# Optimization experiments

Hardware: AMD Instinct MI355X
Metric: run time of the kernel (lower is better)

## Reference

```python
import jax, jax.numpy as jnp
import numpy as np

BN_EPS = 1e-5
ITER_N = 5

def _bn(x, gamma, beta, mean, var, axis):
    shape = [1] * x.ndim
    shape[axis] = -1
    r = lambda v: v.reshape(shape)
    return (x - r(mean)) * (r(gamma) / jnp.sqrt(r(var) + BN_EPS)) + r(beta)

def _covpool(x):
    # x: (B, d, M); MPNCOV CovpoolLayer: y = x @ I_hat @ x^T, I_hat = (1/M)I - (1/M^2)11^T
    M = x.shape[-1]
    I_hat = (-1.0 / (M * M)) * jnp.ones((M, M), x.dtype) + (1.0 / M) * jnp.eye(M, dtype=x.dtype)
    return jnp.einsum('bdm,mn,ben->bde', x, I_hat, x)

def _sqrtm_ns(A, iterN=ITER_N):
    # MPNCOV SqrtmLayer: trace-normalized Newton-Schulz iteration
    d = A.shape[-1]
    I3 = 3.0 * jnp.eye(d, dtype=A.dtype)
    normA = jnp.trace(A, axis1=1, axis2=2) / 3.0          # (B,)
    A_n = A / normA[:, None, None]
    ZY = 0.5 * (I3 - A_n)
    Y = A_n @ ZY
    Z = ZY
    for _ in range(iterN - 2):
        ZY = 0.5 * (I3 - Z @ Y)
        Y = Y @ ZY
        Z = ZY @ Z
    YZY = 0.5 * (Y @ (I3 - Z @ Y))
    return YZY * jnp.sqrt(normA)[:, None, None]

def setup_inputs() -> dict:
    key = jax.random.key(0)
    ks = jax.random.split(key, 12)
    B, C, H, W = 64, 1024, 16, 16
    D, R = 128, H * W  # att_dim, sp_reso
    return {
        'x': jax.random.normal(ks[0], (B, C, H, W), jnp.float32),
        'w_dr': jax.random.normal(ks[1], (D, C), jnp.float32) * 0.02,
        'b_dr': jax.random.normal(ks[2], (D,), jnp.float32) * 0.02,
        'bn1_gamma': jnp.ones((D,), jnp.float32),
        'bn1_beta': jnp.zeros((D,), jnp.float32),
        'bn1_mean': jax.random.normal(ks[3], (D,), jnp.float32) * 0.1,
        'bn1_var': jax.random.uniform(ks[4], (D,), jnp.float32, 0.5, 1.5),
        'bn2_gamma': jnp.ones((R,), jnp.float32),
        'bn2_beta': jnp.zeros((R,), jnp.float32),
        'bn2_mean': jax.random.normal(ks[5], (R,), jnp.float32) * 0.1,
        'bn2_var': jax.random.uniform(ks[6], (R,), jnp.float32, 0.5, 1.5),
        'rc_w': jax.random.normal(ks[7], (R,), jnp.float32) * 0.1 + 1.0,
        'rc_b': jax.random.normal(ks[8], (R,), jnp.float32) * 0.02,
        'fc_w': jax.random.normal(ks[9], (R, R * R), jnp.float32) * 0.004,
        'fc_b': jax.random.normal(ks[10], (R,), jnp.float32) * 0.02,
    }

def reference(x, w_dr, b_dr, bn1_gamma, bn1_beta, bn1_mean, bn1_var,
              bn2_gamma, bn2_beta, bn2_mean, bn2_var, rc_w, rc_b, fc_w, fc_b):
    B, C, H, W = x.shape
    # 1x1 dimension-reduction conv + BN + ReLU
    y = jnp.einsum('bchw,dc->bdhw', x, w_dr) + b_dr[None, :, None, None]
    y = jax.nn.relu(_bn(y, bn1_gamma, bn1_beta, bn1_mean, bn1_var, axis=1))
    # (B, D, HW) -> (B, HW, D): HW spatial positions as 'channels', D as samples
    y = y.reshape(B, -1, H * W).transpose(0, 2, 1)
    cov = _covpool(y)                  # (B, HW, HW)
    s = _sqrtm_ns(cov, ITER_N)         # (B, HW, HW)
    # row BN over first HW axis (channels of the (B, HW, HW, 1) view)
    s = _bn(s, bn2_gamma, bn2_beta, bn2_mean, bn2_var, axis=1)
    # grouped (depthwise) 1x1 row conv: per-row scale + bias
    s = s * rc_w[None, :, None] + rc_b[None, :, None]
    att = jax.nn.sigmoid(s.reshape(B, -1) @ fc_w.T + fc_b)   # (B, HW)
    att = att.reshape(B, 1, H, W)
    return x * att
```

## Files before the change

### kernel.cpp

```cpp
#include <hip/hip_runtime.h>

typedef unsigned short u16;
typedef unsigned int   u32;
typedef __attribute__((ext_vector_type(8))) short bf8;
typedef __attribute__((ext_vector_type(4))) float f4;
typedef __attribute__((ext_vector_type(16))) float f16f;

#define MFMA(a,b,c)   __builtin_amdgcn_mfma_f32_16x16x32_bf16(a,b,c,0,0,0)
#define MFMA32(a,b,c) __builtin_amdgcn_mfma_f32_32x32x16_bf16(a,b,c,0,0,0)

__device__ __forceinline__ u16 f2bf(float f){
  u32 u = __float_as_uint(f);
  u += 0x7fffu + ((u >> 16) & 1u);
  return (u16)(u >> 16);
}
__device__ __forceinline__ float bf2f(u16 h){ return __uint_as_float(((u32)h) << 16); }
__device__ __forceinline__ u32 pk2(float a, float b){ return (u32)f2bf(a) | ((u32)f2bf(b) << 16); }

__device__ __forceinline__ bf8 ldsFrag(const char* m, int row0, int k0, int pitch){
  int l = threadIdx.x & 63;
  int r = row0 + (l & 15);
  int kb = ((k0 + ((l >> 4) << 3)) << 1) ^ ((r & 7) << 4);
  return *(const bf8*)(m + r * pitch + kb);
}
__device__ __forceinline__ void ldsPut(char* m, int row, int col, int pitch, u16 v){
  int kb = (col << 1) ^ ((row & 7) << 4);
  *(u16*)(m + row * pitch + kb) = v;
}

__device__ __forceinline__ bf8 fragNS(const char* m, int r0, int ks, int l){
  int r = r0 + (l & 31);
  int kb = ((ks << 5) + ((l >> 5) << 4)) ^ ((r & 15) << 4);
  return *(const bf8*)(m + r * 256 + kb);
}
__device__ __forceinline__ bf8 fragWT(const char* m, int r0, int ks, int l){
  int r = r0 + (l & 31);
  int kb = ((ks << 5) + ((l >> 5) << 4)) ^ ((r & 15) << 4);
  return *(const bf8*)(m + r * 512 + kb);
}
__device__ __forceinline__ char* nsAddr(char* m, int row, int col4){
  return m + row * 256 + ((col4 << 1) ^ ((row & 15) << 4));
}

__device__ __forceinline__ void mmPass(const char* A, const char* B, f16f (&acc)[2][2],
                                       int R0, int C0, int l){
  #pragma unroll
  for (int ks = 0; ks < 8; ++ks){
    bf8 a0 = fragNS(A, R0,      ks, l);
    bf8 a1 = fragNS(A, R0 + 32, ks, l);
    bf8 b0 = fragNS(B, C0,      ks, l);
    bf8 b1 = fragNS(B, C0 + 32, ks, l);
    acc[0][0] = MFMA32(a0, b0, acc[0][0]); acc[0][1] = MFMA32(a0, b1, acc[0][1]);
    acc[1][0] = MFMA32(a1, b0, acc[1][0]); acc[1][1] = MFMA32(a1, b1, acc[1][1]);
  }
}

__device__ __forceinline__ void writeTile(char* D, const f16f (&acc)[2][2], int R0, int C0, int l,
                                          float scale, float dval, const uint2* adv){
  #pragma unroll
  for (int ri = 0; ri < 2; ++ri)
  #pragma unroll
  for (int ci = 0; ci < 2; ++ci)
  #pragma unroll
  for (int g = 0; g < 4; ++g){
    int srow = C0 + ci * 32 + (l & 31);
    int scol = R0 + ri * 32 + g * 8 + ((l >> 5) << 2);
    float v[4];
    #pragma unroll
    for (int q = 0; q < 4; ++q){
      float x = scale * acc[ri][ci][g * 4 + q];
      x += ((scol + q) == srow) ? dval : 0.f;
      v[q] = x;
    }
    if (adv){
      uint2 ad = adv[(ri * 2 + ci) * 4 + g];
      v[0] += 1.5f * bf2f((u16)ad.x);
      v[1] += 1.5f * bf2f((u16)(ad.x >> 16));
      v[2] += 1.5f * bf2f((u16)ad.y);
      v[3] += 1.5f * bf2f((u16)(ad.y >> 16));
    }
    *(uint2*)nsAddr(D, srow, scol) = make_uint2(pk2(v[0], v[1]), pk2(v[2], v[3]));
  }
}

__global__ void k_zero(float* __restrict__ p){
  int i = blockIdx.x * 256 + threadIdx.x;
  if (i < 16384) p[i] = 0.f;
}

__global__ __launch_bounds__(512) void k_conv(
    const float* __restrict__ x, const float* __restrict__ wdr, const float* __restrict__ bdr,
    const float* __restrict__ g1, const float* __restrict__ be1,
    const float* __restrict__ m1, const float* __restrict__ v1,
    u16* __restrict__ Wg, u16* __restrict__ WTg){
  __shared__ union {
    struct { char A[16384]; char Bt[8192]; } s;
    struct { float y[128 * 65]; float musum[8 * 64]; float mu[64]; } e;
  } sm;
  int t = threadIdx.x;
  int b = blockIdx.x >> 2, hw0 = (blockIdx.x & 3) * 64;
  int w = t >> 6, l = t & 63;
  int rows0 = (w >> 1) * 32, cols0 = (w & 1) * 32;
  int lc = l & 15, lr = (l >> 4) * 4;

  const f4 fz = {0.f, 0.f, 0.f, 0.f};
  f4 acc[2][2];
  acc[0][0] = fz; acc[0][1] = fz; acc[1][0] = fz; acc[1][1] = fz;

  int ad = t >> 2;
  int ac = (t & 3) * 16;
  const float* xb = x + (size_t)b * 1024 * 256 + hw0;

  for (int kk = 0; kk < 16; ++kk) {
    int c0 = kk * 64;
    #pragma unroll
    for (int j = 0; j < 4; ++j) {
      float4 vv = *(const float4*)(wdr + (size_t)ad * 1024 + c0 + ac + j * 4);
      int cb = ((ac + j * 4) * 2) ^ ((ad & 7) << 4);
      *(u32*)(sm.s.A + ad * 128 + cb)     = pk2(vv.x, vv.y);
      *(u32*)(sm.s.A + ad * 128 + cb + 4) = pk2(vv.z, vv.w);
    }
    #pragma unroll
    for (int j2 = 0; j2 < 4; ++j2) {
      int cc = w * 8 + j2 * 2;
      float v0 = xb[(size_t)(c0 + cc) * 256 + l];
      float v1x = xb[(size_t)(c0 + cc + 1) * 256 + l];
      int cb = (cc * 2) ^ ((l & 7) << 4);
      *(u32*)(sm.s.Bt + l * 128 + cb) = pk2(v0, v1x);
    }
    __syncthreads();
    #pragma unroll
    for (int ks = 0; ks < 2; ++ks) {
      int k0 = ks * 32;
      bf8 a0 = ldsFrag(sm.s.A, rows0,      k0, 128);
      bf8 a1 = ldsFrag(sm.s.A, rows0 + 16, k0, 128);
      bf8 b0 = ldsFrag(sm.s.Bt, cols0,      k0, 128);
      bf8 b1 = ldsFrag(sm.s.Bt, cols0 + 16, k0, 128);
      acc[0][0] = MFMA(a0, b0, acc[0][0]);
      acc[0][1] = MFMA(a0, b1, acc[0][1]);
      acc[1][0] = MFMA(a1, b0, acc[1][0]);
      acc[1][1] = MFMA(a1, b1, acc[1][1]);
    }
    __syncthreads();
  }
  #pragma unroll
  for (int i = 0; i < 2; ++i)
    #pragma unroll
    for (int r = 0; r < 4; ++r) {
      int d = rows0 + i * 16 + lr + r;
      float s1 = g1[d] * rsqrtf(v1[d] + 1e-5f);
      float t1 = (bdr[d] - m1[d]) * s1 + be1[d];
      #pragma unroll
      for (int j = 0; j < 2; ++j) {
        int hwl = cols0 + j * 16 + lc;
        sm.e.y[d * 65 + hwl] = fmaxf(acc[i][j][r] * s1 + t1, 0.f);
      }
    }
  __syncthreads();
  { int part = t >> 6, col = t & 63;
    float s = 0.f;
    #pragma unroll
    for (int i2 = 0; i2 < 16; ++i2) s += sm.e.y[(part * 16 + i2) * 65 + col];
    sm.e.musum[part * 64 + col] = s;
  }
  __syncthreads();
  if (t < 64) {
    float m = 0.f;
    #pragma unroll
    for (int p = 0; p < 8; ++p) m += sm.e.musum[p * 64 + t];
    sm.e.mu[t] = m * (1.0f / 128.0f);
  }
  __syncthreads();
  const float ISM = 0.08838834764831845f;
  { int hwl = t >> 3, dc = (t & 7) * 16;
    float muv = sm.e.mu[hwl];
    u32 q[8];
    #pragma unroll
    for (int jj = 0; jj < 8; ++jj) {
      float a = (sm.e.y[(dc + 2 * jj)     * 65 + hwl] - muv) * ISM;
      float c = (sm.e.y[(dc + 2 * jj + 1) * 65 + hwl] - muv) * ISM;
      q[jj] = pk2(a, c);
    }
    uint4* d4 = (uint4*)(Wg + ((size_t)(b * 256 + hw0 + hwl) * 128 + dc));
    d4[0] = make_uint4(q[0], q[1], q[2], q[3]);
    d4[1] = make_uint4(q[4], q[5], q[6], q[7]);
  }
  { int d = t >> 2, hc = (t & 3) * 16;
    u32 q[8];
    #pragma unroll
    for (int jj = 0; jj < 8; ++jj) {
      int h0 = hc + 2 * jj, h1 = hc + 2 * jj + 1;
      float a = (sm.e.y[d * 65 + h0] - sm.e.mu[h0]) * ISM;
      float c = (sm.e.y[d * 65 + h1] - sm.e.mu[h1]) * ISM;
      q[jj] = pk2(a, c);
    }
    uint4* d4 = (uint4*)(WTg + ((size_t)(b * 128 + d) * 256 + hw0 + hc));
    d4[0] = make_uint4(q[0], q[1], q[2], q[3]);
    d4[1] = make_uint4(q[4], q[5], q[6], q[7]);
  }
}

extern __shared__ char smns[];
__global__ __launch_bounds__(512, 2) void k_ns(const u16* __restrict__ WT,
                                               u16* __restrict__ yf, float* __restrict__ normAg){
  int b = blockIdx.x, t = threadIdx.x;
  char* Yb = smns;
  char* Zb = smns + 32768;
  char* T1 = smns + 65536;
  char* T2 = smns + 98304;
  char* T3 = smns + 131072;
  char* WTl = smns + 65536;
  char* G   = T3;
  float* trp = (float*)smns;

  int w = t >> 6, l = t & 63;
  int wq = w & 3;
  int R0 = (wq >> 1) * 64, C0 = (wq & 1) * 64;

  {
    const u16* src = WT + (size_t)b * 32768;
    int row = t >> 2, q = t & 3;
    #pragma unroll
    for (int j = 0; j < 8; ++j) {
      int c16 = q + j * 4;
      bf8 v = *(const bf8*)(src + row * 256 + c16 * 8);
      int ph = c16 ^ (row & 15);
      *(bf8*)(WTl + row * 512 + ph * 16) = v;
    }
  }
  if (t == 0) *trp = 0.f;
  __syncthreads();

  int R0g = (w & 3) * 32, C0g = (w >> 2) * 64;
  const f16f fz16 = {};
  f16f gac[2]; gac[0] = fz16; gac[1] = fz16;
  #pragma unroll
  for (int ks = 0; ks < 16; ++ks){
    bf8 a  = fragWT(WTl, R0g,      ks, l);
    bf8 b0 = fragWT(WTl, C0g,      ks, l);
    bf8 b1 = fragWT(WTl, C0g + 32, ks, l);
    gac[0] = MFMA32(a, b0, gac[0]);
    gac[1] = MFMA32(a, b1, gac[1]);
  }
  float tp = 0.f;
  #pragma unroll
  for (int ci = 0; ci < 2; ++ci)
    #pragma unroll
    for (int e = 0; e < 16; ++e){
      int row = R0g + (e & 3) + 8 * (e >> 2) + ((l >> 5) << 2);
      int col = C0g + ci * 32 + (l & 31);
      if (row == col) tp += gac[ci][e];
    }
  #pragma unroll
  for (int off = 32; off > 0; off >>= 1) tp += __shfl_down(tp, off);
  if (l == 0) atomicAdd(trp, tp);
  __syncthreads();

  float normA = fmaxf(*trp / 3.0f, 1e-12f);
  if (t == 0) normAg[b] = normA;
  float inv = 1.0f / normA;
  #pragma unroll
  for (int ci = 0; ci < 2; ++ci)
    #pragma unroll
    for (int g = 0; g < 4; ++g){
      int srow = C0g + ci * 32 + (l & 31);
      int scol = R0g + g * 8 + ((l >> 5) << 2);
      float v0 = gac[ci][g * 4 + 0] * inv, v1 = gac[ci][g * 4 + 1] * inv;
      float v2 = gac[ci][g * 4 + 2] * inv, v3 = gac[ci][g * 4 + 3] * inv;
      *(uint2*)nsAddr(G, srow, scol) = make_uint2(pk2(v0, v1), pk2(v2, v3));
    }
  __syncthreads();

  bf8 gA[8], gB[8];
  #pragma unroll
  for (int ks = 0; ks < 8; ++ks){
    gA[ks] = fragNS(G, C0,      ks, l);
    gB[ks] = fragNS(G, C0 + 32, ks, l);
  }
  { int row = t >> 2, q4 = t & 3;
    #pragma unroll
    for (int j = 0; j < 4; ++j){
      int c16 = q4 * 4 + j;
      int ph = c16 ^ (row & 15);
      bf8 gg = *(const bf8*)(G + row * 256 + ph * 16);
      bf8 yv, zv;
      #pragma unroll
      for (int e = 0; e < 8; ++e){
        int col = c16 * 8 + e;
        float y = -0.5f * bf2f((u16)gg[e]) + ((col == row) ? 1.5f : 0.f);
        yv[e] = (short)f2bf(y);
        zv[e] = (col == row) ? (short)f2bf(-0.5f) : (short)0;
      }
      *(bf8*)(Yb + row * 256 + ph * 16) = yv;
      *(bf8*)(Zb + row * 256 + ph * 16) = zv;
    }
  }
  __syncthreads();

  float z0 = 1.5f;
  for (int it = 0; it < 4; ++it){
    {
      f16f acc[2][2]; acc[0][0] = fz16; acc[0][1] = fz16; acc[1][0] = fz16; acc[1][1] = fz16;
      const char* As = (w < 4) ? Zb : Yb;
      #pragma unroll
      for (int ks = 0; ks < 8; ++ks){
        bf8 a0 = fragNS(As, R0,      ks, l);
        bf8 a1 = fragNS(As, R0 + 32, ks, l);
        acc[0][0] = MFMA32(a0, gA[ks], acc[0][0]); acc[0][1] = MFMA32(a0, gB[ks], acc[0][1]);
        acc[1][0] = MFMA32(a1, gA[ks], acc[1][0]); acc[1][1] = MFMA32(a1, gB[ks], acc[1][1]);
      }
      writeTile((w < 4) ? T1 : T3, acc, R0, C0, l, 1.0f, (w < 4) ? z0 : 0.f, nullptr);
    }
    __syncthreads();

    uint2 adv[16];
    {
      const char* addsrc = (w < 4) ? Zb : Yb;
      #pragma unroll
      for (int ri = 0; ri < 2; ++ri)
      #pragma unroll
      for (int ci = 0; ci < 2; ++ci)
      #pragma unroll
      for (int g = 0; g < 4; ++g){
        int srow = C0 + ci * 32 + (l & 31);
        int scol = R0 + ri * 32 + g * 8 + ((l >> 5) << 2);
        adv[(ri * 2 + ci) * 4 + g] = *(const uint2*)nsAddr((char*)addsrc, srow, scol);
      }
      if (w < 4){
        f16f acc[2][2]; acc[0][0] = fz16; acc[0][1] = fz16; acc[1][0] = fz16; acc[1][1] = fz16;
        mmPass(T1, Yb, acc, R0, C0, l);
        writeTile(T2, acc, R0, C0, l, -0.5f, 0.f, nullptr);
      }
    }
    __syncthreads();

    if ((w >= 4) || (it < 3)){
      f16f acc[2][2]; acc[0][0] = fz16; acc[0][1] = fz16; acc[1][0] = fz16; acc[1][1] = fz16;
      const char* A3 = (w < 4) ? T2 : T3;
      const char* B3 = (w < 4) ? T1 : T2;
      mmPass(A3, B3, acc, R0, C0, l);
      writeTile((w < 4) ? Zb : Yb, acc, R0, C0, l, 1.0f, 0.f, adv);
    }
    __syncthreads();
    z0 *= 1.5f;
  }

  {
    int row = t >> 2, q = t & 3;
    u16* dst = yf + (size_t)b * 16384 + row * 128;
    #pragma unroll
    for (int j = 0; j < 4; ++j) {
      int c16 = q * 4 + j;
      int ph = c16 ^ (row & 15);
      *(bf8*)(dst + c16 * 8) = *(const bf8*)(Yb + row * 256 + ph * 16);
    }
  }
}

extern __shared__ char smex[];
__global__ __launch_bounds__(512) void k_expand(
    const u16* __restrict__ Wg, const u16* __restrict__ yf, const float* __restrict__ normAg,
    const float* __restrict__ g2, const float* __restrict__ be2, const float* __restrict__ m2,
    const float* __restrict__ v2, const float* __restrict__ rcw, const float* __restrict__ rcb,
    u16* __restrict__ sp){
  int blk = blockIdx.x, b = blk >> 2, iband = blk & 3;
  char* Bm = smex;
  char* Yl = smex + 65536;
  char* El = smex + 98304;
  int t = threadIdx.x;
  { const u16* src = Wg + (size_t)b * 32768;
    int row = t >> 1, q = t & 1;
    #pragma unroll
    for (int j = 0; j < 8; ++j) {
      int c16 = q + j * 2;
      bf8 v = *(const bf8*)(src + row * 128 + c16 * 8);
      int ph = c16 ^ (row & 7);
      *(bf8*)(Bm + row * 256 + ph * 16) = v;
    } }
  { const u16* src = yf + (size_t)b * 16384;
    int row = t >> 2, q = t & 3;
    #pragma unroll
    for (int j = 0; j < 4; ++j) {
      int c16 = q + j * 4;
      bf8 v = *(const bf8*)(src + row * 128 + c16 * 8);
      int ph = c16 ^ (row & 7);
      *(bf8*)(Yl + row * 256 + ph * 16) = v;
    } }
  __syncthreads();
  int w = t >> 6, l = t & 63, lc = l & 15, lr = (l >> 4) * 4;
  const f4 fz = {0.f, 0.f, 0.f, 0.f};
  { int r0 = (w >> 2) * 32, c0 = (w & 3) * 32;
    f4 acc[2][2];
    acc[0][0] = fz; acc[0][1] = fz; acc[1][0] = fz; acc[1][1] = fz;
    #pragma unroll
    for (int kk = 0; kk < 4; ++kk) {
      int k0 = kk * 32;
      bf8 a0 = ldsFrag(Bm, iband * 64 + r0,      k0, 256);
      bf8 a1 = ldsFrag(Bm, iband * 64 + r0 + 16, k0, 256);
      bf8 b0 = ldsFrag(Yl, c0,      k0, 256);
      bf8 b1 = ldsFrag(Yl, c0 + 16, k0, 256);
      acc[0][0] = MFMA(a0, b0, acc[0][0]); acc[0][1] = MFMA(a0, b1, acc[0][1]);
      acc[1][0] = MFMA(a1, b0, acc[1][0]); acc[1][1] = MFMA(a1, b1, acc[1][1]);
    }
    #pragma unroll
    for (int i = 0; i < 2; ++i)
      #pragma unroll
      for (int j = 0; j < 2; ++j)
        #pragma unroll
        for (int r = 0; r < 4; ++r)
          ldsPut(El, r0 + i * 16 + lr + r, c0 + j * 16 + lc, 256, f2bf(acc[i][j][r]));
  }
  __syncthreads();
  { float invs = rsqrtf(normAg[b]);
    int r0 = (w >> 2) * 32, c0 = (w & 3) * 64;
    f4 acc[2][4];
    #pragma unroll
    for (int i = 0; i < 2; ++i)
      #pragma unroll
      for (int j = 0; j < 4; ++j) acc[i][j] = fz;
    #pragma unroll
    for (int kk = 0; kk < 4; ++kk) {
      int k0 = kk * 32;
      bf8 a0 = ldsFrag(El, r0,      k0, 256);
      bf8 a1 = ldsFrag(El, r0 + 16, k0, 256);
      bf8 b0 = ldsFrag(Bm, c0,      k0, 256);
      bf8 b1 = ldsFrag(Bm, c0 + 16, k0, 256);
      bf8 b2 = ldsFrag(Bm, c0 + 32, k0, 256);
      bf8 b3 = ldsFrag(Bm, c0 + 48, k0, 256);
      acc[0][0] = MFMA(a0, b0, acc[0][0]); acc[0][1] = MFMA(a0, b1, acc[0][1]);
      acc[0][2] = MFMA(a0, b2, acc[0][2]); acc[0][3] = MFMA(a0, b3, acc[0][3]);
      acc[1][0] = MFMA(a1, b0, acc[1][0]); acc[1][1] = MFMA(a1, b1, acc[1][1]);
      acc[1][2] = MFMA(a1, b2, acc[1][2]); acc[1][3] = MFMA(a1, b3, acc[1][3]);
    }
    #pragma unroll
    for (int i = 0; i < 2; ++i)
      #pragma unroll
      for (int r = 0; r < 4; ++r) {
        int il = r0 + i * 16 + lr + r;
        int ig = iband * 64 + il;
        float bs = g2[ig] * rsqrtf(v2[ig] + 1e-5f);
        float al = bs * rcw[ig];
        float be = (be2[ig] - m2[ig] * bs) * rcw[ig] + rcb[ig];
        #pragma unroll
        for (int j = 0; j < 4; ++j) {
          int jg = c0 + j * 16 + lc;
          sp[(size_t)b * 65536 + ig * 256 + jg] = f2bf(acc[i][j][r] * invs * al + be);
        }
      }
  }
}

extern __shared__ char smfc[];
__global__ __launch_bounds__(512) void k_fc(const u16* __restrict__ sp,
                                            const float* __restrict__ fcw,
                                            float* __restrict__ logits){
  int kc = blockIdx.x >> 1, rh = blockIdx.x & 1;
  int k0 = kc * 256, rbase = rh * 128;
  char* Al = smfc;
  char* Bl = smfc + 32768;
  int t = threadIdx.x;
  { int row = t >> 3, q = t & 7;
    #pragma unroll
    for (int j = 0; j < 4; ++j) {
      int c16 = q + j * 8;
      bf8 v = *(const bf8*)(sp + (size_t)row * 65536 + k0 + c16 * 8);
      int ph = c16 ^ (row & 7);
      *(bf8*)(Al + row * 512 + ph * 16) = v;
    } }
  { int lane16 = t & 15;
    #pragma unroll
    for (int pass = 0; pass < 4; ++pass) {
      int row = (t >> 4) + pass * 32;
      #pragma unroll
      for (int j = 0; j < 4; ++j) {
        int k = lane16 * 4 + j * 64;
        float4 v = *(const float4*)(fcw + (size_t)(rbase + row) * 65536 + k0 + k);
        int off = (k * 2) ^ ((row & 7) << 4);
        *(u32*)(Bl + row * 512 + off)     = pk2(v.x, v.y);
        *(u32*)(Bl + row * 512 + off + 4) = pk2(v.z, v.w);
      }
    } }
  __syncthreads();
  int w = t >> 6, l = t & 63, lc = l & 15, lr = (l >> 4) * 4;
  int r0 = (w >> 2) * 32, c0 = (w & 3) * 32;
  const f4 fz = {0.f, 0.f, 0.f, 0.f};
  f4 acc[2][2];
  acc[0][0] = fz; acc[0][1] = fz; acc[1][0] = fz; acc[1][1] = fz;
  #pragma unroll
  for (int kk = 0; kk < 8; ++kk) {
    int ks = kk * 32;
    bf8 a0 = ldsFrag(Al, r0,      ks, 512);
    bf8 a1 = ldsFrag(Al, r0 + 16, ks, 512);
    bf8 b0 = ldsFrag(Bl, c0,      ks, 512);
    bf8 b1 = ldsFrag(Bl, c0 + 16, ks, 512);
    acc[0][0] = MFMA(a0, b0, acc[0][0]); acc[0][1] = MFMA(a0, b1, acc[0][1]);
    acc[1][0] = MFMA(a1, b0, acc[1][0]); acc[1][1] = MFMA(a1, b1, acc[1][1]);
  }
  #pragma unroll
  for (int i = 0; i < 2; ++i)
    #pragma unroll
    for (int j = 0; j < 2; ++j)
      #pragma unroll
      for (int r = 0; r < 4; ++r) {
        int row = r0 + i * 16 + lr + r;
        int col = rbase + c0 + j * 16 + lc;
        atomicAdd(logits + row * 256 + col, acc[i][j][r]);
      }
}

__global__ __launch_bounds__(256) void k_mul(const float* __restrict__ x,
                                             const float* __restrict__ logits,
                                             const float* __restrict__ fcb,
                                             float* __restrict__ out, int n4){
  int i = blockIdx.x * 256 + threadIdx.x;
  int str = gridDim.x * 256;
  for (; i < n4; i += str) {
    int e = i << 2;
    int b = e >> 18;
    int hw = e & 255;
    float4 xv = ((const float4*)x)[i];
    float4 lg = *(const float4*)(logits + (b << 8) + hw);
    float4 fb = *(const float4*)(fcb + hw);
    float4 o;
    o.x = xv.x / (1.f + expf(-(lg.x + fb.x)));
    o.y = xv.y / (1.f + expf(-(lg.y + fb.y)));
    o.z = xv.z / (1.f + expf(-(lg.z + fb.z)));
    o.w = xv.w / (1.f + expf(-(lg.w + fb.w)));
    ((float4*)out)[i] = o;
  }
}

extern "C" void kernel_launch(void* const* d_in, const int* in_sizes, int n_in,
                              void* d_out, int out_size, void* d_ws, size_t ws_size,
                              hipStream_t stream){
  const float* x   = (const float*)d_in[0];
  const float* wdr = (const float*)d_in[1];
  const float* bdr = (const float*)d_in[2];
  const float* g1  = (const float*)d_in[3];
  const float* be1 = (const float*)d_in[4];
  const float* m1  = (const float*)d_in[5];
  const float* v1  = (const float*)d_in[6];
  const float* g2  = (const float*)d_in[7];
  const float* be2 = (const float*)d_in[8];
  const float* m2  = (const float*)d_in[9];
  const float* v2  = (const float*)d_in[10];
  const float* rcw = (const float*)d_in[11];
  const float* rcb = (const float*)d_in[12];
  const float* fcw = (const float*)d_in[13];
  const float* fcb = (const float*)d_in[14];
  float* out = (float*)d_out;
  char* ws = (char*)d_ws;
  u16*   Wg  = (u16*)(ws);
  u16*   WTg = (u16*)(ws + (4u  << 20));
  u16*   yfg = (u16*)(ws + (8u  << 20));
  float* nAg = (float*)(ws + (10u << 20));
  u16*   spg = (u16*)(ws + (11u << 20));
  float* lgt = (float*)(ws + (20u << 20));

  hipFuncSetAttribute((const void*)k_ns,     hipFuncAttributeMaxDynamicSharedMemorySize, 163840);
  hipFuncSetAttribute((const void*)k_expand, hipFuncAttributeMaxDynamicSharedMemorySize, 114688);
  hipFuncSetAttribute((const void*)k_fc,     hipFuncAttributeMaxDynamicSharedMemorySize, 98304);

  k_zero  <<<64,   256, 0,      stream>>>(lgt);
  k_conv  <<<256,  512, 0,      stream>>>(x, wdr, bdr, g1, be1, m1, v1, Wg, WTg);
  k_ns    <<<64,   512, 163840, stream>>>(WTg, yfg, nAg);
  k_expand<<<256,  512, 114688, stream>>>(Wg, yfg, nAg, g2, be2, m2, v2, rcw, rcb, spg);
  k_fc    <<<512,  512, 98304,  stream>>>(spg, fcw, lgt);
  k_mul   <<<2048, 256, 0,      stream>>>(x, lgt, fcb, out, 4194304);
}
```

Measured before the change: 122.1 us.

## Pre-convert conv weights to swizzled bf16, double-buffer conv loads, halve spatial tile

A new prep kernel converts the 1x1 conv weight to bf16 in the swizzled LDS layout once per call and also zeroes the logits buffer. The conv kernel now copies those prepped weights straight into LDS and prefetches the next K-chunk of weights and input into registers while the MFMAs run on double-buffered LDS. Each block covers 32 spatial positions instead of 64, doubling the grid to 512 blocks for better CU occupancy. The cost is that every block rereads the full weight tile, and the grid adds an extra round of per-block epilogue reductions.

```diff
diff --git a/kernel.cpp b/kernel.cpp
--- a/kernel.cpp
+++ b/kernel.cpp
@@ -83,120 +83,133 @@
   }
 }
 
-__global__ void k_zero(float* __restrict__ p){
+__global__ __launch_bounds__(256) void k_prep(const float* __restrict__ wdr,
+                                              float* __restrict__ logits,
+                                              u16* __restrict__ prep){
   int i = blockIdx.x * 256 + threadIdx.x;
-  if (i < 16384) p[i] = 0.f;
+  if (i < 16384) logits[i] = 0.f;
+  #pragma unroll
+  for (int j = 0; j < 2; ++j){
+    int e = i + j * 65536;
+    int chunk = e >> 13, rem = e & 8191, d = rem >> 6, cb2 = rem & 63;
+    int c = ((cb2 * 2) ^ ((d & 7) << 4)) >> 1;
+    prep[e] = f2bf(wdr[d * 1024 + chunk * 64 + c]);
+  }
 }
 
 __global__ __launch_bounds__(512) void k_conv(
-    const float* __restrict__ x, const float* __restrict__ wdr, const float* __restrict__ bdr,
+    const u16* __restrict__ wprep, const float* __restrict__ x, const float* __restrict__ bdr,
     const float* __restrict__ g1, const float* __restrict__ be1,
     const float* __restrict__ m1, const float* __restrict__ v1,
     u16* __restrict__ Wg, u16* __restrict__ WTg){
   __shared__ union {
-    struct { char A[16384]; char Bt[8192]; } s;
-    struct { float y[128 * 65]; float musum[8 * 64]; float mu[64]; } e;
+    struct { u16 A[2][8192]; u16 Bt[2][2048]; } s;
+    struct { float y[128 * 33]; float musum[512]; float mu[32]; } e;
   } sm;
   int t = threadIdx.x;
-  int b = blockIdx.x >> 2, hw0 = (blockIdx.x & 3) * 64;
+  int b = blockIdx.x >> 3, hw0 = (blockIdx.x & 7) * 32;
+  const float* xb = x + (size_t)b * 262144 + hw0;
+
   int w = t >> 6, l = t & 63;
-  int rows0 = (w >> 1) * 32, cols0 = (w & 1) * 32;
+  int d0 = (w >> 1) * 32, hh = (w & 1) * 16;
   int lc = l & 15, lr = (l >> 4) * 4;
 
   const f4 fz = {0.f, 0.f, 0.f, 0.f};
-  f4 acc[2][2];
-  acc[0][0] = fz; acc[0][1] = fz; acc[1][0] = fz; acc[1][1] = fz;
-
-  int ad = t >> 2;
-  int ac = (t & 3) * 16;
-  const float* xb = x + (size_t)b * 1024 * 256 + hw0;
-
-  for (int kk = 0; kk < 16; ++kk) {
-    int c0 = kk * 64;
-    #pragma unroll
-    for (int j = 0; j < 4; ++j) {
-      float4 vv = *(const float4*)(wdr + (size_t)ad * 1024 + c0 + ac + j * 4);
-      int cb = ((ac + j * 4) * 2) ^ ((ad & 7) << 4);
-      *(u32*)(sm.s.A + ad * 128 + cb)     = pk2(vv.x, vv.y);
-      *(u32*)(sm.s.A + ad * 128 + cb + 4) = pk2(vv.z, vv.w);
-    }
-    #pragma unroll
-    for (int j2 = 0; j2 < 4; ++j2) {
-      int cc = w * 8 + j2 * 2;
-      float v0 = xb[(size_t)(c0 + cc) * 256 + l];
-      float v1x = xb[(size_t)(c0 + cc + 1) * 256 + l];
-      int cb = (cc * 2) ^ ((l & 7) << 4);
-      *(u32*)(sm.s.Bt + l * 128 + cb) = pk2(v0, v1x);
+  f4 acc[2]; acc[0] = fz; acc[1] = fz;
+
+  int cp = t >> 5, hwl = t & 31;
+
+  uint4 ar0, ar1;
+  float br0, br1, br2, br3;
+  { const uint4* s4 = (const uint4*)wprep;
+    ar0 = s4[t]; ar1 = s4[t + 512];
+    br0 = xb[(size_t)(2 * cp)      * 256 + hwl];
+    br1 = xb[(size_t)(2 * cp + 1)  * 256 + hwl];
+    br2 = xb[(size_t)(2 * cp + 32) * 256 + hwl];
+    br3 = xb[(size_t)(2 * cp + 33) * 256 + hwl];
+  }
+
+  for (int k = 0; k < 16; ++k){
+    int cur = k & 1;
+    *(uint4*)(sm.s.A[cur] + t * 8)        = ar0;
+    *(uint4*)(sm.s.A[cur] + 4096 + t * 8) = ar1;
+    { int b0 = (4 * cp) ^ ((hwl & 7) << 4);
+      int b1 = (4 * cp + 64) ^ ((hwl & 7) << 4);
+      *(u32*)((char*)sm.s.Bt[cur] + hwl * 128 + b0) = pk2(br0, br1);
+      *(u32*)((char*)sm.s.Bt[cur] + hwl * 128 + b1) = pk2(br2, br3);
     }
     __syncthreads();
-    #pragma unroll
-    for (int ks = 0; ks < 2; ++ks) {
+    if (k < 15){
+      const uint4* s4 = (const uint4*)(wprep + (k + 1) * 8192);
+      ar0 = s4[t]; ar1 = s4[t + 512];
+      int c0 = (k + 1) * 64;
+      br0 = xb[(size_t)(c0 + 2 * cp)      * 256 + hwl];
+      br1 = xb[(size_t)(c0 + 2 * cp + 1)  * 256 + hwl];
+      br2 = xb[(size_t)(c0 + 2 * cp + 32) * 256 + hwl];
+      br3 = xb[(size_t)(c0 + 2 * cp + 33) * 256 + hwl];
+    }
+    #pragma unroll
+    for (int ks = 0; ks < 2; ++ks){
       int k0 = ks * 32;
-      bf8 a0 = ldsFrag(sm.s.A, rows0,      k0, 128);
-      bf8 a1 = ldsFrag(sm.s.A, rows0 + 16, k0, 128);
-      bf8 b0 = ldsFrag(sm.s.Bt, cols0,      k0, 128);
-      bf8 b1 = ldsFrag(sm.s.Bt, cols0 + 16, k0, 128);
-      acc[0][0] = MFMA(a0, b0, acc[0][0]);
-      acc[0][1] = MFMA(a0, b1, acc[0][1]);
-      acc[1][0] = MFMA(a1, b0, acc[1][0]);
-      acc[1][1] = MFMA(a1, b1, acc[1][1]);
+      bf8 a0 = ldsFrag((const char*)sm.s.A[cur], d0,      k0, 128);
+      bf8 a1 = ldsFrag((const char*)sm.s.A[cur], d0 + 16, k0, 128);
+      bf8 b0 = ldsFrag((const char*)sm.s.Bt[cur], hh, k0, 128);
+      acc[0] = MFMA(a0, b0, acc[0]);
+      acc[1] = MFMA(a1, b0, acc[1]);
     }
     __syncthreads();
   }
+
   #pragma unroll
   for (int i = 0; i < 2; ++i)
     #pragma unroll
-    for (int r = 0; r < 4; ++r) {
-      int d = rows0 + i * 16 + lr + r;
+    for (int r = 0; r < 4; ++r){
+      int d = d0 + i * 16 + lr + r;
       float s1 = g1[d] * rsqrtf(v1[d] + 1e-5f);
       float t1 = (bdr[d] - m1[d]) * s1 + be1[d];
-      #pragma unroll
-      for (int j = 0; j < 2; ++j) {
-        int hwl = cols0 + j * 16 + lc;
-        sm.e.y[d * 65 + hwl] = fmaxf(acc[i][j][r] * s1 + t1, 0.f);
-      }
-    }
-  __syncthreads();
-  { int part = t >> 6, col = t & 63;
+      int hwp = hh + lc;
+      sm.e.y[d * 33 + hwp] = fmaxf(acc[i][r] * s1 + t1, 0.f);
+    }
+  __syncthreads();
+  {
+    int part = t >> 5, col = t & 31;
     float s = 0.f;
     #pragma unroll
-    for (int i2 = 0; i2 < 16; ++i2) s += sm.e.y[(part * 16 + i2) * 65 + col];
-    sm.e.musum[part * 64 + col] = s;
-  }
-  __syncthreads();
-  if (t < 64) {
+    for (int i2 = 0; i2 < 8; ++i2) s += sm.e.y[(part * 8 + i2) * 33 + col];
+    sm.e.musum[part * 32 + col] = s;
+  }
+  __syncthreads();
+  if (t < 32){
     float m = 0.f;
     #pragma unroll
-    for (int p = 0; p < 8; ++p) m += sm.e.musum[p * 64 + t];
+    for (int p = 0; p < 16; ++p) m += sm.e.musum[p * 32 + t];
     sm.e.mu[t] = m * (1.0f / 128.0f);
   }
   __syncthreads();
   const float ISM = 0.08838834764831845f;
-  { int hwl = t >> 3, dc = (t & 7) * 16;
-    float muv = sm.e.mu[hwl];
-    u32 q[8];
-    #pragma unroll
-    for (int jj = 0; jj < 8; ++jj) {
-      float a = (sm.e.y[(dc + 2 * jj)     * 65 + hwl] - muv) * ISM;
-      float c = (sm.e.y[(dc + 2 * jj + 1) * 65 + hwl] - muv) * ISM;
+  {
+    int hwp = t >> 4, dc = (t & 15) * 8;
+    float muv = sm.e.mu[hwp];
+    u32 q[4];
+    #pragma unroll
+    for (int jj = 0; jj < 4; ++jj){
+      float a = (sm.e.y[(dc + 2 * jj)     * 33 + hwp] - muv) * ISM;
+      float c = (sm.e.y[(dc + 2 * jj + 1) * 33 + hwp] - muv) * ISM;
       q[jj] = pk2(a, c);
     }
-    uint4* d4 = (uint4*)(Wg + ((size_t)(b * 256 + hw0 + hwl) * 128 + dc));
-    d4[0] = make_uint4(q[0], q[1], q[2], q[3]);
-    d4[1] = make_uint4(q[4], q[5], q[6], q[7]);
-  }
-  { int d = t >> 2, hc = (t & 3) * 16;
-    u32 q[8];
-    #pragma unroll
-    for (int jj = 0; jj < 8; ++jj) {
+    *(uint4*)(Wg + ((size_t)(b * 256 + hw0 + hwp) * 128 + dc)) = make_uint4(q[0], q[1], q[2], q[3]);
+  }
+  {
+    int d = t >> 2, hc = (t & 3) * 8;
+    u32 q[4];
+    #pragma unroll
+    for (int jj = 0; jj < 4; ++jj){
       int h0 = hc + 2 * jj, h1 = hc + 2 * jj + 1;
-      float a = (sm.e.y[d * 65 + h0] - sm.e.mu[h0]) * ISM;
-      float c = (sm.e.y[d * 65 + h1] - sm.e.mu[h1]) * ISM;
+      float a = (sm.e.y[d * 33 + h0] - sm.e.mu[h0]) * ISM;
+      float c = (sm.e.y[d * 33 + h1] - sm.e.mu[h1]) * ISM;
       q[jj] = pk2(a, c);
     }
-    uint4* d4 = (uint4*)(WTg + ((size_t)(b * 128 + d) * 256 + hw0 + hc));
-    d4[0] = make_uint4(q[0], q[1], q[2], q[3]);
-    d4[1] = make_uint4(q[4], q[5], q[6], q[7]);
+    *(uint4*)(WTg + ((size_t)(b * 128 + d) * 256 + hw0 + hc)) = make_uint4(q[0], q[1], q[2], q[3]);
   }
 }
 
@@ -217,8 +230,7 @@
   int wq = w & 3;
   int R0 = (wq >> 1) * 64, C0 = (wq & 1) * 64;
 
-  {
-    const u16* src = WT + (size_t)b * 32768;
+  { const u16* src = WT + (size_t)b * 32768;
     int row = t >> 2, q = t & 3;
     #pragma unroll
     for (int j = 0; j < 8; ++j) {
@@ -345,8 +357,7 @@
     z0 *= 1.5f;
   }
 
-  {
-    int row = t >> 2, q = t & 3;
+  { int row = t >> 2, q = t & 3;
     u16* dst = yf + (size_t)b * 16384 + row * 128;
     #pragma unroll
     for (int j = 0; j < 4; ++j) {
@@ -554,6 +565,7 @@
   u16*   WTg = (u16*)(ws + (4u  << 20));
   u16*   yfg = (u16*)(ws + (8u  << 20));
   float* nAg = (float*)(ws + (10u << 20));
+  u16*   wpr = (u16*)(ws + (10u << 20) + 4096);
   u16*   spg = (u16*)(ws + (11u << 20));
   float* lgt = (float*)(ws + (20u << 20));
 
@@ -561,8 +573,8 @@
   hipFuncSetAttribute((const void*)k_expand, hipFuncAttributeMaxDynamicSharedMemorySize, 114688);
   hipFuncSetAttribute((const void*)k_fc,     hipFuncAttributeMaxDynamicSharedMemorySize, 98304);
 
-  k_zero  <<<64,   256, 0,      stream>>>(lgt);
-  k_conv  <<<256,  512, 0,      stream>>>(x, wdr, bdr, g1, be1, m1, v1, Wg, WTg);
+  k_prep  <<<256,  256, 0,      stream>>>(wdr, lgt, wpr);
+  k_conv  <<<512,  512, 0,      stream>>>(wpr, x, bdr, g1, be1, m1, v1, Wg, WTg);
   k_ns    <<<64,   512, 163840, stream>>>(WTg, yfg, nAg);
   k_expand<<<256,  512, 114688, stream>>>(Wg, yfg, nAg, g2, be2, m2, v2, rcw, rcb, spg);
   k_fc    <<<512,  512, 98304,  stream>>>(spg, fcw, lgt);
```

New measurement: 115.7 us. -5.3%, faster.
